# Performance work log

Hardware: AMD Instinct MI355X
Metric: run time of the kernel (lower is better)

The kernel has to match this reference:

```python
import jax, jax.numpy as jnp
import numpy as np

N = 50000          # num vertices
K = 16             # max padded neighbors
D = 256            # feature dim
H = 256            # num_hidddens


def setup_inputs() -> dict:
    key = jax.random.key(0)
    k1, k2, k3, k4, k5 = jax.random.split(key, 5)
    vertex_feat = jax.random.normal(k1, (N, D), dtype=jnp.float32)
    neighbors_idx = jax.random.randint(k2, (N, K), 0, N, dtype=jnp.int32)
    valid_lens = jax.random.randint(k3, (N,), 0, K + 1, dtype=jnp.int32)
    W = jax.random.normal(k4, (D, H), dtype=jnp.float32) * (1.0 / np.sqrt(D))
    B = jax.random.normal(k5, (D, H), dtype=jnp.float32) * (1.0 / np.sqrt(D))
    return {"vertex_feat": vertex_feat, "neighbors_idx": neighbors_idx,
            "valid_lens": valid_lens, "W": W, "B": B}


def reference(vertex_feat, neighbors_idx, valid_lens, W, B):
    # gather neighbor features: [N, K, D]
    nb = vertex_feat[neighbors_idx]
    # sequence mask over padded neighbor slots: [N, K]
    mask = (jnp.arange(K)[None, :] < valid_lens[:, None]).astype(vertex_feat.dtype)
    # masked sum then mean (valid_lens==0 -> divide by 1, matching tf.where guard)
    agg = jnp.einsum('nkd,nk->nd', nb, mask)
    denom = jnp.maximum(valid_lens, 1).astype(vertex_feat.dtype)
    agg = agg / denom[:, None]
    # dual dense (no bias) + relu
    out = jax.nn.relu(agg @ W + vertex_feat @ B)
    return out
```

## Files before the change

### kernel.cpp

```cpp
#include <hip/hip_runtime.h>
#include <hip/hip_bf16.h>
#include <stdint.h>


#define N_V   50000
#define KNB   16
#define D_F   256
#define H_F   256
#define K2    512
#define NPAD  50048

typedef __bf16 bf16x8 __attribute__((ext_vector_type(8)));
typedef float  f32x4  __attribute__((ext_vector_type(4)));

static __device__ __forceinline__ unsigned short f2bf(float f) {
    union { float f; unsigned u; } v; v.f = f;
    unsigned u = v.u;
    u += 0x7fffu + ((u >> 16) & 1u);
    return (unsigned short)(u >> 16);
}

static __device__ __forceinline__ void load16(const void* g, void* l) {
    __builtin_amdgcn_global_load_lds(
        (__attribute__((address_space(1))) void*)g,
        (__attribute__((address_space(3))) void*)l, 16, 0, 0);
}

__global__ __launch_bounds__(256) void wb_convert(
    const float* __restrict__ W, const float* __restrict__ Bm,
    unsigned short* __restrict__ WBt) {
    int t = blockIdx.x * 256 + threadIdx.x;
    int h = t >> 9;
    int k = t & 511;
    float v = (k < 256) ? W[(size_t)k * H_F + h]
                        : Bm[(size_t)(k - 256) * H_F + h];
    WBt[t] = f2bf(v);
}

__global__ __launch_bounds__(256) void gather_mean(
    const float* __restrict__ vf, const int* __restrict__ nbr,
    const int* __restrict__ lens, unsigned short* __restrict__ Abuf) {
    int wave = threadIdx.x >> 6;
    int lane = threadIdx.x & 63;
    int n = blockIdx.x * 4 + wave;
    if (n >= NPAD) return;
    unsigned short* arow = Abuf + (size_t)n * K2;
    if (n >= N_V) {
        ushort4 z = {0, 0, 0, 0};
        ((ushort4*)arow)[lane] = z;
        ((ushort4*)(arow + 256))[lane] = z;
        return;
    }
    int len = lens[n];
    const int* nb = nbr + (size_t)n * KNB;
    float4 acc = make_float4(0.f, 0.f, 0.f, 0.f);
    for (int k = 0; k < len; ++k) {
        int j = __builtin_amdgcn_readfirstlane(nb[k]);
        const float4 v = ((const float4*)(vf + (size_t)j * D_F))[lane];
        acc.x += v.x; acc.y += v.y; acc.z += v.z; acc.w += v.w;
    }
    float inv = 1.0f / (float)(len > 0 ? len : 1);
    ushort4 o;
    o.x = f2bf(acc.x * inv); o.y = f2bf(acc.y * inv);
    o.z = f2bf(acc.z * inv); o.w = f2bf(acc.w * inv);
    ((ushort4*)arow)[lane] = o;
    const float4 v = ((const float4*)(vf + (size_t)n * D_F))[lane];
    ushort4 o2;
    o2.x = f2bf(v.x); o2.y = f2bf(v.y); o2.z = f2bf(v.z); o2.w = f2bf(v.w);
    ((ushort4*)(arow + 256))[lane] = o2;
}

__global__ __launch_bounds__(256) void gemm_relu(
    const unsigned short* __restrict__ Abuf,
    const unsigned short* __restrict__ WBt,
    float* __restrict__ out) {
    __shared__ char Alds[8192];
    __shared__ char Blds[8192];
    const int bn = blockIdx.x * 128;
    const int bm = blockIdx.y * 128;
    const int tid  = threadIdx.x;
    const int wave = tid >> 6, lane = tid & 63;
    const int wm = wave >> 1, wn = wave & 1;

    f32x4 acc[4][4];
    const f32x4 fzero = {0.f, 0.f, 0.f, 0.f};
#pragma unroll
    for (int i = 0; i < 4; ++i)
#pragma unroll
        for (int j = 0; j < 4; ++j) acc[i][j] = fzero;

    const char* Ab = (const char*)(Abuf + (size_t)bm * K2);
    const char* Bb = (const char*)(WBt + (size_t)bn * K2);

    for (int k0 = 0; k0 < K2; k0 += 32) {
        __syncthreads();
#pragma unroll
        for (int i = 0; i < 2; ++i) {
            unsigned P = i * 4096 + tid * 16;
            unsigned L = P ^ (((P >> 6) & 3u) << 4);
            unsigned row = L >> 6;
            unsigned colb = L & 63u;
            const char* ga = Ab + (size_t)row * (K2 * 2) + k0 * 2 + colb;
            const char* gb = Bb + (size_t)row * (K2 * 2) + k0 * 2 + colb;
            char* la = Alds + i * 4096 + wave * 1024;
            char* lb = Blds + i * 4096 + wave * 1024;
            load16(ga, la);
            load16(gb, lb);
        }
        __syncthreads();

        bf16x8 af[4], bfr[4];
#pragma unroll
        for (int mf = 0; mf < 4; ++mf) {
            unsigned r = wm * 64 + mf * 16 + (lane & 15);
            unsigned L = r * 64 + ((lane >> 4) << 4);
            unsigned P = L ^ (((L >> 6) & 3u) << 4);
            af[mf] = *(const bf16x8*)(Alds + P);
        }
#pragma unroll
        for (int nf = 0; nf < 4; ++nf) {
            unsigned r = wn * 64 + nf * 16 + (lane & 15);
            unsigned L = r * 64 + ((lane >> 4) << 4);
            unsigned P = L ^ (((L >> 6) & 3u) << 4);
            bfr[nf] = *(const bf16x8*)(Blds + P);
        }
#pragma unroll
        for (int mf = 0; mf < 4; ++mf)
#pragma unroll
            for (int nf = 0; nf < 4; ++nf)
                acc[mf][nf] = __builtin_amdgcn_mfma_f32_16x16x32_bf16(
                    af[mf], bfr[nf], acc[mf][nf], 0, 0, 0);
    }

#pragma unroll
    for (int mf = 0; mf < 4; ++mf) {
        int row0 = bm + wm * 64 + mf * 16 + ((lane >> 4) << 2);
#pragma unroll
        for (int nf = 0; nf < 4; ++nf) {
            int col = bn + wn * 64 + nf * 16 + (lane & 15);
            f32x4 v = acc[mf][nf];
#pragma unroll
            for (int i = 0; i < 4; ++i) {
                int row = row0 + i;
                if (row < N_V)
                    out[(size_t)row * H_F + col] = fmaxf(v[i], 0.0f);
            }
        }
    }
}

extern "C" void kernel_launch(void* const* d_in, const int* in_sizes, int n_in,
                              void* d_out, int out_size, void* d_ws, size_t ws_size,
                              hipStream_t stream) {
    const float* vf   = (const float*)d_in[0];
    const int*   nbr  = (const int*)d_in[1];
    const int*   lens = (const int*)d_in[2];
    const float* W    = (const float*)d_in[3];
    const float* Bm   = (const float*)d_in[4];
    float* out = (float*)d_out;

    unsigned short* Abuf = (unsigned short*)d_ws;
    unsigned short* WBt  = (unsigned short*)((char*)d_ws +
                             (size_t)NPAD * K2 * sizeof(unsigned short));

    hipLaunchKernelGGL(wb_convert, dim3(512), dim3(256), 0, stream, W, Bm, WBt);
    hipLaunchKernelGGL(gather_mean, dim3(NPAD / 4), dim3(256), 0, stream,
                       vf, nbr, lens, Abuf);
    hipLaunchKernelGGL(gemm_relu, dim3(2, NPAD / 128), dim3(256), 0, stream,
                       Abuf, WBt, out);
}
```

Baseline: 194.5 us.

## Pre-convert features to bf16, gather bf16 rows, double-buffer full-N GEMM tiles

Adds a pass that converts vertex features to bf16 once, so the gather reads half as many bytes per neighbor. The gather now loads neighbor indices with one coalesced load, broadcasts them by shuffle, and unrolls by four for memory-level parallelism. The GEMM block covers all 256 output columns with 512 threads and double-buffered LDS, reading A directly from the aggregated and converted buffers. The W/B transpose uses an LDS tile for coalescing. The cost is an extra full pass over vertex_feat, and neighbor sums are now taken from bf16-rounded inputs.

Result: faster. 167.3 us (-14.0%).

```diff
diff --git a/kernel.cpp b/kernel.cpp
--- a/kernel.cpp
+++ b/kernel.cpp
@@ -1,5 +1,4 @@
 #include <hip/hip_runtime.h>
-#include <hip/hip_bf16.h>
 #include <stdint.h>
 
 
@@ -12,6 +11,7 @@
 
 typedef __bf16 bf16x8 __attribute__((ext_vector_type(8)));
 typedef float  f32x4  __attribute__((ext_vector_type(4)));
+typedef unsigned short ushort8 __attribute__((ext_vector_type(8)));
 
 static __device__ __forceinline__ unsigned short f2bf(float f) {
     union { float f; unsigned u; } v; v.f = f;
@@ -19,68 +19,113 @@
     u += 0x7fffu + ((u >> 16) & 1u);
     return (unsigned short)(u >> 16);
 }
-
+static __device__ __forceinline__ float bf2f(unsigned short u) {
+    union { unsigned u; float f; } v; v.u = ((unsigned)u) << 16; return v.f;
+}
 static __device__ __forceinline__ void load16(const void* g, void* l) {
     __builtin_amdgcn_global_load_lds(
         (__attribute__((address_space(1))) void*)g,
         (__attribute__((address_space(3))) void*)l, 16, 0, 0);
 }
 
-__global__ __launch_bounds__(256) void wb_convert(
+__global__ __launch_bounds__(256) void vf_convert(
+    const float* __restrict__ vf, unsigned short* __restrict__ vfb) {
+    const int total = NPAD * (D_F / 8);
+    for (int c = blockIdx.x * 256 + threadIdx.x; c < total; c += gridDim.x * 256) {
+        int n = c >> 5;
+        int off = (c & 31) * 8;
+        ushort8 o;
+        if (n < N_V) {
+            const float4 a = *(const float4*)(vf + (size_t)n * D_F + off);
+            const float4 b = *(const float4*)(vf + (size_t)n * D_F + off + 4);
+            o[0]=f2bf(a.x); o[1]=f2bf(a.y); o[2]=f2bf(a.z); o[3]=f2bf(a.w);
+            o[4]=f2bf(b.x); o[5]=f2bf(b.y); o[6]=f2bf(b.z); o[7]=f2bf(b.w);
+        } else {
+            o = (ushort8)(0);
+        }
+        *(ushort8*)(vfb + (size_t)n * D_F + off) = o;
+    }
+}
+
+__global__ __launch_bounds__(256) void wbt_convert(
     const float* __restrict__ W, const float* __restrict__ Bm,
     unsigned short* __restrict__ WBt) {
-    int t = blockIdx.x * 256 + threadIdx.x;
-    int h = t >> 9;
-    int k = t & 511;
-    float v = (k < 256) ? W[(size_t)k * H_F + h]
-                        : Bm[(size_t)(k - 256) * H_F + h];
-    WBt[t] = f2bf(v);
+    __shared__ unsigned short t[32][34];
+    const int k0 = blockIdx.x * 32;
+    const int h0 = blockIdx.y * 32;
+    const int tid = threadIdx.x;
+    {
+        int r  = tid >> 3;
+        int c4 = (tid & 7) * 4;
+        int kg = k0 + r;
+        const float* src = (kg < 256) ? (W  + (size_t)kg * H_F + h0 + c4)
+                                      : (Bm + (size_t)(kg - 256) * H_F + h0 + c4);
+        float4 v = *(const float4*)src;
+        t[r][c4 + 0] = f2bf(v.x); t[r][c4 + 1] = f2bf(v.y);
+        t[r][c4 + 2] = f2bf(v.z); t[r][c4 + 3] = f2bf(v.w);
+    }
+    __syncthreads();
+    {
+        int hh  = tid >> 3;
+        int kk4 = (tid & 7) * 4;
+        ushort4 o;
+        o.x = t[kk4 + 0][hh]; o.y = t[kk4 + 1][hh];
+        o.z = t[kk4 + 2][hh]; o.w = t[kk4 + 3][hh];
+        *(ushort4*)(WBt + (size_t)(h0 + hh) * K2 + k0 + kk4) = o;
+    }
 }
 
 __global__ __launch_bounds__(256) void gather_mean(
-    const float* __restrict__ vf, const int* __restrict__ nbr,
-    const int* __restrict__ lens, unsigned short* __restrict__ Abuf) {
-    int wave = threadIdx.x >> 6;
-    int lane = threadIdx.x & 63;
-    int n = blockIdx.x * 4 + wave;
+    const unsigned short* __restrict__ vfb, const int* __restrict__ nbr,
+    const int* __restrict__ lens, unsigned short* __restrict__ aggb) {
+    const int wave = threadIdx.x >> 6;
+    const int lane = threadIdx.x & 63;
+    const int n = blockIdx.x * 4 + wave;
     if (n >= NPAD) return;
-    unsigned short* arow = Abuf + (size_t)n * K2;
+    unsigned short* arow = aggb + (size_t)n * D_F;
     if (n >= N_V) {
         ushort4 z = {0, 0, 0, 0};
-        ((ushort4*)arow)[lane] = z;
-        ((ushort4*)(arow + 256))[lane] = z;
+        *(ushort4*)(arow + lane * 4) = z;
         return;
     }
-    int len = lens[n];
-    const int* nb = nbr + (size_t)n * KNB;
-    float4 acc = make_float4(0.f, 0.f, 0.f, 0.f);
-    for (int k = 0; k < len; ++k) {
-        int j = __builtin_amdgcn_readfirstlane(nb[k]);
-        const float4 v = ((const float4*)(vf + (size_t)j * D_F))[lane];
-        acc.x += v.x; acc.y += v.y; acc.z += v.z; acc.w += v.w;
-    }
-    float inv = 1.0f / (float)(len > 0 ? len : 1);
+    const int len = lens[n];
+    const int idx = nbr[(size_t)n * KNB + (lane & 15)];
+    f32x4 acc = {0.f, 0.f, 0.f, 0.f};
+#define ROW_(j) (*(const ushort4*)(vfb + (size_t)(j) * D_F + lane * 4))
+#define ACC_(v) { acc[0] += bf2f(v.x); acc[1] += bf2f(v.y); \
+                  acc[2] += bf2f(v.z); acc[3] += bf2f(v.w); }
+    int k = 0;
+    for (; k + 4 <= len; k += 4) {
+        int j0 = __shfl(idx, k),     j1 = __shfl(idx, k + 1);
+        int j2 = __shfl(idx, k + 2), j3 = __shfl(idx, k + 3);
+        ushort4 v0 = ROW_(j0), v1 = ROW_(j1), v2 = ROW_(j2), v3 = ROW_(j3);
+        ACC_(v0); ACC_(v1); ACC_(v2); ACC_(v3);
+    }
+    for (; k < len; ++k) {
+        int j = __shfl(idx, k);
+        ushort4 v = ROW_(j);
+        ACC_(v);
+    }
+#undef ROW_
+#undef ACC_
+    const float inv = 1.0f / (float)(len > 0 ? len : 1);
     ushort4 o;
-    o.x = f2bf(acc.x * inv); o.y = f2bf(acc.y * inv);
-    o.z = f2bf(acc.z * inv); o.w = f2bf(acc.w * inv);
-    ((ushort4*)arow)[lane] = o;
-    const float4 v = ((const float4*)(vf + (size_t)n * D_F))[lane];
-    ushort4 o2;
-    o2.x = f2bf(v.x); o2.y = f2bf(v.y); o2.z = f2bf(v.z); o2.w = f2bf(v.w);
-    ((ushort4*)(arow + 256))[lane] = o2;
-}
-
-__global__ __launch_bounds__(256) void gemm_relu(
-    const unsigned short* __restrict__ Abuf,
+    o.x = f2bf(acc[0] * inv); o.y = f2bf(acc[1] * inv);
+    o.z = f2bf(acc[2] * inv); o.w = f2bf(acc[3] * inv);
+    *(ushort4*)(arow + lane * 4) = o;
+}
+
+__global__ __launch_bounds__(512) void gemm_relu(
+    const unsigned short* __restrict__ aggb,
+    const unsigned short* __restrict__ vfb,
     const unsigned short* __restrict__ WBt,
     float* __restrict__ out) {
-    __shared__ char Alds[8192];
-    __shared__ char Blds[8192];
-    const int bn = blockIdx.x * 128;
-    const int bm = blockIdx.y * 128;
+    __shared__ char Alds[2][8192];
+    __shared__ char Blds[2][16384];
+    const int bm = blockIdx.x * 128;
     const int tid  = threadIdx.x;
     const int wave = tid >> 6, lane = tid & 63;
-    const int wm = wave >> 1, wn = wave & 1;
+    const int wm = wave >> 2, wn = wave & 3;
 
     f32x4 acc[4][4];
     const f32x4 fzero = {0.f, 0.f, 0.f, 0.f};
@@ -89,40 +134,46 @@
 #pragma unroll
         for (int j = 0; j < 4; ++j) acc[i][j] = fzero;
 
-    const char* Ab = (const char*)(Abuf + (size_t)bm * K2);
-    const char* Bb = (const char*)(WBt + (size_t)bn * K2);
-
-    for (int k0 = 0; k0 < K2; k0 += 32) {
-        __syncthreads();
+    auto stage = [&](int buf, int t) {
+        const int k0 = t * 32;
+        {
+            unsigned P = tid * 16u;
+            unsigned L = P ^ (((P >> 6) & 3u) << 4);
+            unsigned row = L >> 6, colb = L & 63u;
+            const char* src = (k0 < 256)
+                ? (const char*)aggb + (size_t)(bm + row) * 512 + k0 * 2 + colb
+                : (const char*)vfb  + (size_t)(bm + row) * 512 + (k0 - 256) * 2 + colb;
+            load16(src, Alds[buf] + wave * 1024);
+        }
 #pragma unroll
         for (int i = 0; i < 2; ++i) {
-            unsigned P = i * 4096 + tid * 16;
+            unsigned P = i * 8192u + tid * 16u;
             unsigned L = P ^ (((P >> 6) & 3u) << 4);
-            unsigned row = L >> 6;
-            unsigned colb = L & 63u;
-            const char* ga = Ab + (size_t)row * (K2 * 2) + k0 * 2 + colb;
-            const char* gb = Bb + (size_t)row * (K2 * 2) + k0 * 2 + colb;
-            char* la = Alds + i * 4096 + wave * 1024;
-            char* lb = Blds + i * 4096 + wave * 1024;
-            load16(ga, la);
-            load16(gb, lb);
-        }
-        __syncthreads();
-
+            unsigned row = L >> 6, colb = L & 63u;
+            const char* src = (const char*)WBt + (size_t)row * 1024 + k0 * 2 + colb;
+            load16(src, Blds[buf] + i * 8192 + wave * 1024);
+        }
+    };
+
+    stage(0, 0);
+    __syncthreads();
+    int cur = 0;
+    for (int t = 0; t < 16; ++t) {
+        if (t < 15) stage(cur ^ 1, t + 1);
         bf16x8 af[4], bfr[4];
 #pragma unroll
         for (int mf = 0; mf < 4; ++mf) {
             unsigned r = wm * 64 + mf * 16 + (lane & 15);
             unsigned L = r * 64 + ((lane >> 4) << 4);
             unsigned P = L ^ (((L >> 6) & 3u) << 4);
-            af[mf] = *(const bf16x8*)(Alds + P);
+            af[mf] = *(const bf16x8*)(Alds[cur] + P);
         }
 #pragma unroll
         for (int nf = 0; nf < 4; ++nf) {
             unsigned r = wn * 64 + nf * 16 + (lane & 15);
             unsigned L = r * 64 + ((lane >> 4) << 4);
             unsigned P = L ^ (((L >> 6) & 3u) << 4);
-            bfr[nf] = *(const bf16x8*)(Blds + P);
+            bfr[nf] = *(const bf16x8*)(Blds[cur] + P);
         }
 #pragma unroll
         for (int mf = 0; mf < 4; ++mf)
@@ -130,6 +181,8 @@
             for (int nf = 0; nf < 4; ++nf)
                 acc[mf][nf] = __builtin_amdgcn_mfma_f32_16x16x32_bf16(
                     af[mf], bfr[nf], acc[mf][nf], 0, 0, 0);
+        __syncthreads();
+        cur ^= 1;
     }
 
 #pragma unroll
@@ -137,7 +190,7 @@
         int row0 = bm + wm * 64 + mf * 16 + ((lane >> 4) << 2);
 #pragma unroll
         for (int nf = 0; nf < 4; ++nf) {
-            int col = bn + wn * 64 + nf * 16 + (lane & 15);
+            int col = wn * 64 + nf * 16 + (lane & 15);
             f32x4 v = acc[mf][nf];
 #pragma unroll
             for (int i = 0; i < 4; ++i) {
@@ -159,13 +212,14 @@
     const float* Bm   = (const float*)d_in[4];
     float* out = (float*)d_out;
 
-    unsigned short* Abuf = (unsigned short*)d_ws;
-    unsigned short* WBt  = (unsigned short*)((char*)d_ws +
-                             (size_t)NPAD * K2 * sizeof(unsigned short));
-
-    hipLaunchKernelGGL(wb_convert, dim3(512), dim3(256), 0, stream, W, Bm, WBt);
+    unsigned short* aggb = (unsigned short*)d_ws;
+    unsigned short* vfb  = aggb + (size_t)NPAD * D_F;
+    unsigned short* WBt  = vfb + (size_t)NPAD * D_F;
+
+    hipLaunchKernelGGL(vf_convert, dim3(2048), dim3(256), 0, stream, vf, vfb);
+    hipLaunchKernelGGL(wbt_convert, dim3(16, 8), dim3(256), 0, stream, W, Bm, WBt);
     hipLaunchKernelGGL(gather_mean, dim3(NPAD / 4), dim3(256), 0, stream,
-                       vf, nbr, lens, Abuf);
-    hipLaunchKernelGGL(gemm_relu, dim3(2, NPAD / 128), dim3(256), 0, stream,
-                       Abuf, WBt, out);
-}
+                       vfb, nbr, lens, aggb);
+    hipLaunchKernelGGL(gemm_relu, dim3(NPAD / 128), dim3(512), 0, stream,
+                       aggb, vfb, WBt, out);
+}
```
